# Kernel optimization log

Hardware: AMD Instinct MI355X
Metric: run time of the kernel (lower is better)

## Reference

```python
import jax, jax.numpy as jnp
import numpy as np

D, H, E, K, DFF = 1024, 16, 8, 2, 4096
B, L, T = 4, 512, 2048
EPS = 1e-5


def _xavier(key, shape):
    fan_in, fan_out = shape[-1], shape[-2]
    a = jnp.sqrt(6.0 / (fan_in + fan_out))
    return jax.random.uniform(key, shape, jnp.float32, -a, a)


def setup_inputs() -> dict:
    key = jax.random.key(0)
    ks = jax.random.split(key, 16)
    inp = {
        'latents': jax.random.normal(ks[0], (B, L, D), jnp.float32),
        'tokens': jax.random.normal(ks[1], (B, T, D), jnp.float32),
        # self-attn
        'sa_ln_g': jnp.ones((D,)), 'sa_ln_b': jnp.zeros((D,)),
        'sa_in_w': _xavier(ks[2], (3 * D, D)), 'sa_in_b': jnp.zeros((3 * D,)),
        'sa_out_w': _xavier(ks[3], (D, D)), 'sa_out_b': jnp.zeros((D,)),
        # cross-attn
        'ca_q_ln_g': jnp.ones((D,)), 'ca_q_ln_b': jnp.zeros((D,)),
        'ca_kv_ln_g': jnp.ones((D,)), 'ca_kv_ln_b': jnp.zeros((D,)),
        'ca_in_w': _xavier(ks[4], (3 * D, D)), 'ca_in_b': jnp.zeros((3 * D,)),
        'ca_out_w': _xavier(ks[5], (D, D)), 'ca_out_b': jnp.zeros((D,)),
        # FuseMoE
        'moe_ln_g': jnp.ones((D,)), 'moe_ln_b': jnp.zeros((D,)),
        'router_w': _xavier(ks[6], (E, D)), 'router_b': jnp.zeros((E,)),
        'e_fc1_w': jax.vmap(lambda k: _xavier(k, (DFF, D)))(jax.random.split(ks[7], E)),
        'e_fc1_b': jnp.zeros((E, DFF)),
        'e_fc2_w': jax.vmap(lambda k: _xavier(k, (D, DFF)))(jax.random.split(ks[8], E)),
        'e_fc2_b': jnp.zeros((E, D)),
    }
    return inp


def _ln(x, g, b):
    m = x.mean(-1, keepdims=True)
    v = ((x - m) ** 2).mean(-1, keepdims=True)
    return (x - m) / jnp.sqrt(v + EPS) * g + b


def _mha(q_in, kv_in, in_w, in_b, out_w, out_b):
    # torch nn.MultiheadAttention (batch_first, no masks, eval)
    wq, wk, wv = jnp.split(in_w, 3, axis=0)
    bq, bk, bv = jnp.split(in_b, 3, axis=0)
    dh = D // H
    def heads(x, w, b):  # [B,S,D] -> [B,H,S,dh]
        y = x @ w.T + b
        return y.reshape(x.shape[0], x.shape[1], H, dh).transpose(0, 2, 1, 3)
    q = heads(q_in, wq, bq)
    k = heads(kv_in, wk, bk)
    v = heads(kv_in, wv, bv)
    scores = jnp.einsum('bhqd,bhkd->bhqk', q, k) / jnp.sqrt(jnp.float32(dh))
    attn = jax.nn.softmax(scores, axis=-1)
    out = jnp.einsum('bhqk,bhkd->bhqd', attn, v)
    out = out.transpose(0, 2, 1, 3).reshape(q_in.shape[0], q_in.shape[1], D)
    return out @ out_w.T + out_b


def _fuse_moe(x, ln_g, ln_b, rw, rb, fc1_w, fc1_b, fc2_w, fc2_b):
    h = _ln(x, ln_g, ln_b)
    logits = h @ rw.T + rb                      # [B,L,E]
    vals, idx = jax.lax.top_k(logits, K)        # [B,L,K]
    gates = jax.nn.softmax(vals, axis=-1)
    N = x.shape[0] * x.shape[1]
    hf = h.reshape(N, D)
    # dense all-expert FFN (faithful to original)
    h1 = jax.nn.gelu(jnp.einsum('nd,efd->enf', hf, fc1_w) + fc1_b[:, None, :], approximate=False)
    eo = jnp.einsum('enf,edf->end', h1, fc2_w) + fc2_b[:, None, :]  # [E,N,D]
    idx_f = idx.reshape(N, K)
    gates_f = gates.reshape(N, K)
    gathered = eo[idx_f, jnp.arange(N)[:, None], :]  # [N,K,D]
    mixed = (gathered * gates_f[..., None]).sum(axis=1).reshape(x.shape)
    return x + mixed


def reference(latents, tokens, sa_ln_g, sa_ln_b, sa_in_w, sa_in_b, sa_out_w, sa_out_b,
              ca_q_ln_g, ca_q_ln_b, ca_kv_ln_g, ca_kv_ln_b, ca_in_w, ca_in_b, ca_out_w, ca_out_b,
              moe_ln_g, moe_ln_b, router_w, router_b, e_fc1_w, e_fc1_b, e_fc2_w, e_fc2_b):
    # self-attn (pre-LN, q=k=v)
    q = _ln(latents, sa_ln_g, sa_ln_b)
    x = latents + _mha(q, q, sa_in_w, sa_in_b, sa_out_w, sa_out_b)
    # cross-attn
    qc = _ln(x, ca_q_ln_g, ca_q_ln_b)
    kv = _ln(tokens, ca_kv_ln_g, ca_kv_ln_b)
    x = x + _mha(qc, kv, ca_in_w, ca_in_b, ca_out_w, ca_out_b)
    # FuseMoE FFN
    return _fuse_moe(x, moe_ln_g, moe_ln_b, router_w, router_b, e_fc1_w, e_fc1_b, e_fc2_w, e_fc2_b)
```

## Files before the change

### kernel.cpp

```cpp
#include <hip/hip_runtime.h>
#include <hip/hip_bf16.h>
#include <math.h>

typedef __hip_bfloat16 bf16;
typedef __bf16 bf16x8v __attribute__((ext_vector_type(8)));
typedef float f32x4 __attribute__((ext_vector_type(4)));
typedef unsigned short us8v __attribute__((ext_vector_type(8)));

#define DD   1024
#define HH   16
#define DHD  64
#define EE   8
#define BB   4
#define LL   512
#define TT   2048
#define DFFD 4096
#define NLAT 2048
#define NTOK 8192
#define NASG 4096

__device__ __forceinline__ float toF(float x) { return x; }
__device__ __forceinline__ float toF(bf16 x) { return __bfloat162float(x); }
__device__ __forceinline__ float us2f(unsigned short u) {
    union { unsigned int i; float f; } v; v.i = ((unsigned int)u) << 16; return v.f;
}
__device__ __forceinline__ unsigned short f2us(float f) {
    bf16 t = __float2bfloat16(f);
    return *(unsigned short*)&t;
}

__device__ __forceinline__ float block_sum256(float val, float* red) {
    #pragma unroll
    for (int off = 32; off > 0; off >>= 1) val += __shfl_down(val, off);
    if ((threadIdx.x & 63) == 0) red[threadIdx.x >> 6] = val;
    __syncthreads();
    if (threadIdx.x == 0) red[4] = red[0] + red[1] + red[2] + red[3];
    __syncthreads();
    float r = red[4];
    __syncthreads();
    return r;
}

__global__ __launch_bounds__(256) void ln_kernel(
    const float* __restrict__ x, const float* __restrict__ g, const float* __restrict__ b,
    bf16* __restrict__ out)
{
    __shared__ float red[5];
    int row = blockIdx.x;
    int tid = threadIdx.x;
    const float* xr = x + (size_t)row * DD;
    float v[4];
    #pragma unroll
    for (int i = 0; i < 4; ++i) v[i] = xr[tid + i * 256];
    float s = v[0] + v[1] + v[2] + v[3];
    float mean = block_sum256(s, red) * (1.0f / DD);
    float sq = 0.f;
    #pragma unroll
    for (int i = 0; i < 4; ++i) { float d = v[i] - mean; sq += d * d; }
    float var = block_sum256(sq, red) * (1.0f / DD);
    float rstd = rsqrtf(var + 1e-5f);
    bf16* orow = out + (size_t)row * DD;
    #pragma unroll
    for (int i = 0; i < 4; ++i) {
        int c = tid + i * 256;
        orow[c] = __float2bfloat16((v[i] - mean) * rstd * g[c] + b[c]);
    }
}

__global__ __launch_bounds__(256) void mfma_gemm_kernel(
    const bf16* __restrict__ A, const float* __restrict__ W,
    const float* __restrict__ bias,
    bf16* __restrict__ Cb, float* __restrict__ Cf,
    int M, int N, int K,
    const float* __restrict__ res, int act, int split,
    const int* __restrict__ gather,
    const int* __restrict__ seg_off, const int* __restrict__ seg_cnt)
{
    int m_base = 0, mrows = M;
    if (seg_off) {
        int e = blockIdx.z;
        m_base = seg_off[e];
        mrows  = seg_cnt[e];
        W    += (size_t)e * N * K;
        bias += (size_t)e * N;
    }
    const int m0 = blockIdx.y * 128;
    if (m0 >= mrows) return;
    const int n0 = blockIdx.x * 128;

    __shared__ bf16 As[4][128][8];
    __shared__ bf16 Wh[4][128][8];
    __shared__ bf16 Wl[4][128][8];

    const int tid  = threadIdx.x;
    const int wid  = tid >> 6;
    const int lane = tid & 63;
    const int lg   = lane >> 4;
    const int l16  = lane & 15;
    const int mb   = (wid >> 1) * 64;
    const int nb   = (wid & 1) * 64;

    const int srow  = tid >> 1;
    const int shalf = tid & 1;
    const int kg0   = shalf * 2;

    const bool a_ok = (m0 + srow) < mrows;
    const unsigned short* aptr = nullptr;
    if (a_ok) {
        int grow = m_base + m0 + srow;
        int asrc = gather ? gather[grow] : grow;
        aptr = (const unsigned short*)(A + (size_t)asrc * K + shalf * 16);
    }
    const float* wptr = W + (size_t)(n0 + srow) * K + shalf * 16;

    f32x4 acc[4][4] = {};

    for (int k0 = 0; k0 < K; k0 += 32) {
        us8v av0 = {0,0,0,0,0,0,0,0}, av1 = {0,0,0,0,0,0,0,0};
        if (a_ok) {
            av0 = *(const us8v*)(aptr + k0);
            av1 = *(const us8v*)(aptr + k0 + 8);
        }
        float4 w0 = *(const float4*)(wptr + k0);
        float4 w1 = *(const float4*)(wptr + k0 + 4);
        float4 w2 = *(const float4*)(wptr + k0 + 8);
        float4 w3 = *(const float4*)(wptr + k0 + 12);

        us8v hi0, hi1, lo0, lo1;
        {
            const float fw[16] = {w0.x, w0.y, w0.z, w0.w, w1.x, w1.y, w1.z, w1.w,
                                  w2.x, w2.y, w2.z, w2.w, w3.x, w3.y, w3.z, w3.w};
            #pragma unroll
            for (int j = 0; j < 8; ++j) {
                unsigned short h0 = f2us(fw[j]);
                unsigned short h1 = f2us(fw[j + 8]);
                hi0[j] = h0; hi1[j] = h1;
                lo0[j] = f2us(fw[j] - us2f(h0));
                lo1[j] = f2us(fw[j + 8] - us2f(h1));
            }
        }
        *(us8v*)&As[kg0][srow][0]     = av0;
        *(us8v*)&As[kg0 + 1][srow][0] = av1;
        *(us8v*)&Wh[kg0][srow][0]     = hi0;
        *(us8v*)&Wh[kg0 + 1][srow][0] = hi1;
        if (split) {
            *(us8v*)&Wl[kg0][srow][0]     = lo0;
            *(us8v*)&Wl[kg0 + 1][srow][0] = lo1;
        }
        __syncthreads();

        bf16x8v af[4], wf[4];
        #pragma unroll
        for (int i = 0; i < 4; ++i) af[i] = *(const bf16x8v*)&As[lg][mb + i * 16 + l16][0];
        if (split) {
            bf16x8v wlf[4];
            #pragma unroll
            for (int j = 0; j < 4; ++j) wlf[j] = *(const bf16x8v*)&Wl[lg][nb + j * 16 + l16][0];
            #pragma unroll
            for (int i = 0; i < 4; ++i)
                #pragma unroll
                for (int j = 0; j < 4; ++j)
                    acc[i][j] = __builtin_amdgcn_mfma_f32_16x16x32_bf16(af[i], wlf[j], acc[i][j], 0, 0, 0);
        }
        #pragma unroll
        for (int j = 0; j < 4; ++j) wf[j] = *(const bf16x8v*)&Wh[lg][nb + j * 16 + l16][0];
        #pragma unroll
        for (int i = 0; i < 4; ++i)
            #pragma unroll
            for (int j = 0; j < 4; ++j)
                acc[i][j] = __builtin_amdgcn_mfma_f32_16x16x32_bf16(af[i], wf[j], acc[i][j], 0, 0, 0);
        __syncthreads();
    }

    #pragma unroll
    for (int i = 0; i < 4; ++i) {
        #pragma unroll
        for (int r = 0; r < 4; ++r) {
            int mm = m0 + mb + i * 16 + lg * 4 + r;
            if (mm >= mrows) continue;
            size_t crow = (size_t)(m_base + mm);
            #pragma unroll
            for (int j = 0; j < 4; ++j) {
                int nn = n0 + nb + j * 16 + l16;
                float v = acc[i][j][r] + bias[nn];
                if (act == 1) v = 0.5f * v * (1.0f + erff(v * 0.70710678118654752f));
                if (res) v += res[crow * (size_t)N + nn];
                if (Cb) Cb[crow * (size_t)N + nn] = __float2bfloat16(v);
                else    Cf[crow * (size_t)N + nn] = v;
            }
        }
    }
}

__global__ __launch_bounds__(256) void attn_mfma_kernel(
    const bf16* __restrict__ Q, int ldq, int qoff,
    const bf16* __restrict__ KV, int ldk, int koff, int voff,
    bf16* __restrict__ O, int Lq, int Tk)
{
    __shared__ bf16 Qs[64][72];
    __shared__ bf16 Ks[32][72];
    __shared__ bf16 Vs[64][40];
    __shared__ bf16 Psh[4][16][40];
    __shared__ bf16 Psl[4][16][40];

    const int nqb = Lq >> 6;
    const int qb  = blockIdx.x % nqb;
    const int h   = (blockIdx.x / nqb) % HH;
    const int b   = blockIdx.x / (nqb * HH);

    const int tid  = threadIdx.x;
    const int wq   = tid >> 6;
    const int lane = tid & 63;
    const int lg   = lane >> 4;
    const int l16  = lane & 15;

    {
        const int row = tid >> 2;
        const int c0  = (tid & 3) * 16;
        const unsigned short* src = (const unsigned short*)
            (Q + (size_t)(b * Lq + qb * 64 + row) * ldq + qoff + h * DHD + c0);
        #pragma unroll
        for (int hf = 0; hf < 2; ++hf) {
            us8v v = *(const us8v*)(src + hf * 8);
            us8v o;
            #pragma unroll
            for (int j = 0; j < 8; ++j) o[j] = f2us(us2f(v[j]) * 0.125f);
            *(us8v*)&Qs[row][c0 + hf * 8] = o;
        }
    }
    __syncthreads();

    const int qrow = wq * 16 + l16;
    const bf16x8v fQ0 = *(const bf16x8v*)&Qs[qrow][lg * 8];
    const bf16x8v fQ1 = *(const bf16x8v*)&Qs[qrow][32 + lg * 8];

    float m = -1e30f, lsum = 0.f;
    f32x4 Of[4] = {};

    const size_t kvbase = (size_t)b * Tk * ldk;
    const int kst_k = tid >> 3;
    const int kst_c = (tid & 7) * 8;
    const int vst_k = (tid & 15) * 2;
    const int vst_d = (tid >> 4) * 4;

    for (int t0 = 0; t0 < Tk; t0 += 32) {
        {
            const bf16* ks = KV + kvbase + (size_t)(t0 + kst_k) * ldk + koff + h * DHD + kst_c;
            *(float4*)&Ks[kst_k][kst_c] = *(const float4*)ks;
        }
        {
            const bf16* vsrc = KV + kvbase + (size_t)(t0 + vst_k) * ldk + voff + h * DHD + vst_d;
            ushort4 a = *(const ushort4*)vsrc;
            ushort4 c = *(const ushort4*)(vsrc + ldk);
            unsigned int w;
            w = (unsigned)a.x | ((unsigned)c.x << 16); *(unsigned*)&Vs[vst_d + 0][vst_k] = w;
            w = (unsigned)a.y | ((unsigned)c.y << 16); *(unsigned*)&Vs[vst_d + 1][vst_k] = w;
            w = (unsigned)a.z | ((unsigned)c.z << 16); *(unsigned*)&Vs[vst_d + 2][vst_k] = w;
            w = (unsigned)a.w | ((unsigned)c.w << 16); *(unsigned*)&Vs[vst_d + 3][vst_k] = w;
        }
        __syncthreads();

        f32x4 st0 = {}, st1 = {};
        {
            const bf16x8v k00 = *(const bf16x8v*)&Ks[l16][lg * 8];
            const bf16x8v k10 = *(const bf16x8v*)&Ks[16 + l16][lg * 8];
            const bf16x8v k01 = *(const bf16x8v*)&Ks[l16][32 + lg * 8];
            const bf16x8v k11 = *(const bf16x8v*)&Ks[16 + l16][32 + lg * 8];
            st0 = __builtin_amdgcn_mfma_f32_16x16x32_bf16(k00, fQ0, st0, 0, 0, 0);
            st1 = __builtin_amdgcn_mfma_f32_16x16x32_bf16(k10, fQ0, st1, 0, 0, 0);
            st0 = __builtin_amdgcn_mfma_f32_16x16x32_bf16(k01, fQ1, st0, 0, 0, 0);
            st1 = __builtin_amdgcn_mfma_f32_16x16x32_bf16(k11, fQ1, st1, 0, 0, 0);
        }

        float cm = fmaxf(fmaxf(fmaxf(st0[0], st0[1]), fmaxf(st0[2], st0[3])),
                         fmaxf(fmaxf(st1[0], st1[1]), fmaxf(st1[2], st1[3])));
        cm = fmaxf(cm, __shfl_xor(cm, 16));
        cm = fmaxf(cm, __shfl_xor(cm, 32));
        const float nm = fmaxf(m, cm);
        float p0[4], p1[4];
        float ps = 0.f;
        #pragma unroll
        for (int r = 0; r < 4; ++r) { p0[r] = expf(st0[r] - nm); ps += p0[r]; }
        #pragma unroll
        for (int r = 0; r < 4; ++r) { p1[r] = expf(st1[r] - nm); ps += p1[r]; }
        ps += __shfl_xor(ps, 16);
        ps += __shfl_xor(ps, 32);
        const float alpha = expf(m - nm);
        lsum = lsum * alpha + ps;
        m = nm;

        ushort4 h0, h1, lo0, lo1;
        #pragma unroll
        for (int r = 0; r < 4; ++r) {
            unsigned short hh = f2us(p0[r]);
            ((unsigned short*)&h0)[r]  = hh;
            ((unsigned short*)&lo0)[r] = f2us(p0[r] - us2f(hh));
        }
        #pragma unroll
        for (int r = 0; r < 4; ++r) {
            unsigned short hh = f2us(p1[r]);
            ((unsigned short*)&h1)[r]  = hh;
            ((unsigned short*)&lo1)[r] = f2us(p1[r] - us2f(hh));
        }
        *(ushort4*)&Psh[wq][l16][lg * 4]      = h0;
        *(ushort4*)&Psh[wq][l16][16 + lg * 4] = h1;
        *(ushort4*)&Psl[wq][l16][lg * 4]      = lo0;
        *(ushort4*)&Psl[wq][l16][16 + lg * 4] = lo1;

        #pragma unroll
        for (int r = 0; r < 4; ++r) {
            const float ar = __shfl(alpha, lg * 4 + r);
            Of[0][r] *= ar; Of[1][r] *= ar; Of[2][r] *= ar; Of[3][r] *= ar;
        }

        __syncthreads();

        const bf16x8v pah = *(const bf16x8v*)&Psh[wq][l16][lg * 8];
        const bf16x8v pal = *(const bf16x8v*)&Psl[wq][l16][lg * 8];
        #pragma unroll
        for (int bb = 0; bb < 4; ++bb) {
            const bf16x8v bv = *(const bf16x8v*)&Vs[bb * 16 + l16][lg * 8];
            Of[bb] = __builtin_amdgcn_mfma_f32_16x16x32_bf16(pal, bv, Of[bb], 0, 0, 0);
            Of[bb] = __builtin_amdgcn_mfma_f32_16x16x32_bf16(pah, bv, Of[bb], 0, 0, 0);
        }
        __syncthreads();
    }

    #pragma unroll
    for (int r = 0; r < 4; ++r) {
        const float inv = 1.0f / __shfl(lsum, lg * 4 + r);
        const int grow = b * Lq + qb * 64 + wq * 16 + lg * 4 + r;
        bf16* orow = O + (size_t)grow * DD + h * DHD;
        #pragma unroll
        for (int bb = 0; bb < 4; ++bb)
            orow[bb * 16 + l16] = __float2bfloat16(Of[bb][r] * inv);
    }
}

__global__ __launch_bounds__(64) void router_kernel(
    const float* __restrict__ X2,
    const float* __restrict__ g, const float* __restrict__ b,
    const float* __restrict__ rw, const float* __restrict__ rb,
    float* __restrict__ gates, int* __restrict__ ebuf, int* __restrict__ counts)
{
    int n = blockIdx.x;
    int lane = threadIdx.x;
    const float* xr = X2 + (size_t)n * DD;

    float v[16];
    #pragma unroll
    for (int i = 0; i < 16; ++i) v[i] = xr[lane + i * 64];

    float s = 0.f;
    #pragma unroll
    for (int i = 0; i < 16; ++i) s += v[i];
    #pragma unroll
    for (int off = 32; off > 0; off >>= 1) s += __shfl_xor(s, off);
    float mean = s * (1.0f / DD);

    float sq = 0.f;
    #pragma unroll
    for (int i = 0; i < 16; ++i) { float d = v[i] - mean; sq += d * d; }
    #pragma unroll
    for (int off = 32; off > 0; off >>= 1) sq += __shfl_xor(sq, off);
    float rstd = rsqrtf(sq * (1.0f / DD) + 1e-5f);

    float h[16];
    #pragma unroll
    for (int i = 0; i < 16; ++i) {
        int c = lane + i * 64;
        h[i] = (v[i] - mean) * rstd * g[c] + b[c];
    }

    float logit[EE];
    #pragma unroll
    for (int e = 0; e < EE; ++e) {
        const float* wr = rw + (size_t)e * DD;
        float p = 0.f;
        #pragma unroll
        for (int i = 0; i < 16; ++i) p += h[i] * wr[lane + i * 64];
        #pragma unroll
        for (int off = 32; off > 0; off >>= 1) p += __shfl_xor(p, off);
        logit[e] = p;
    }

    if (lane == 0) {
        #pragma unroll
        for (int e = 0; e < EE; ++e) logit[e] += rb[e];
        int i0 = 0;
        #pragma unroll
        for (int e = 1; e < EE; ++e) if (logit[e] > logit[i0]) i0 = e;
        int i1 = -1;
        #pragma unroll
        for (int e = 0; e < EE; ++e) {
            if (e == i0) continue;
            if (i1 < 0 || logit[e] > logit[i1]) i1 = e;
        }
        float ex = expf(logit[i1] - logit[i0]);
        float inv = 1.0f / (1.0f + ex);
        gates[2 * n + 0] = inv;
        gates[2 * n + 1] = ex * inv;
        ebuf[2 * n + 0] = i0;
        ebuf[2 * n + 1] = i1;
        atomicAdd(&counts[i0], 1);
        atomicAdd(&counts[i1], 1);
    }
}

__global__ void zero8_kernel(int* __restrict__ p) {
    if (threadIdx.x < EE) p[threadIdx.x] = 0;
}

__global__ void prefix_kernel(const int* __restrict__ counts,
                              int* __restrict__ seg_off, int* __restrict__ cursors) {
    if (threadIdx.x == 0) {
        int acc = 0;
        for (int e = 0; e < EE; ++e) { seg_off[e] = acc; cursors[e] = acc; acc += counts[e]; }
    }
}

__global__ __launch_bounds__(256) void scatter_kernel(
    const int* __restrict__ ebuf, int* __restrict__ cursors,
    int* __restrict__ tok_list, int* __restrict__ r_of)
{
    int n = blockIdx.x * 256 + threadIdx.x;
    if (n < NLAT) {
        for (int k = 0; k < 2; ++k) {
            int e = ebuf[2 * n + k];
            int r = atomicAdd(&cursors[e], 1);
            tok_list[r] = n;
            r_of[2 * n + k] = r;
        }
    }
}

__global__ __launch_bounds__(256) void mix_kernel(
    const float* __restrict__ X2, const bf16* __restrict__ EOUT,
    const float* __restrict__ gates, const int* __restrict__ r_of,
    float* __restrict__ out)
{
    int id = blockIdx.x * 256 + threadIdx.x;
    int n = id >> 10;
    int d = id & 1023;
    float v = X2[id]
            + gates[2 * n + 0] * toF(EOUT[(size_t)r_of[2 * n + 0] * DD + d])
            + gates[2 * n + 1] * toF(EOUT[(size_t)r_of[2 * n + 1] * DD + d]);
    out[id] = v;
}

extern "C" void kernel_launch(void* const* d_in, const int* in_sizes, int n_in,
                              void* d_out, int out_size, void* d_ws, size_t ws_size,
                              hipStream_t stream)
{
    const float* latents  = (const float*)d_in[0];
    const float* tokens   = (const float*)d_in[1];
    const float* sa_ln_g  = (const float*)d_in[2];
    const float* sa_ln_b  = (const float*)d_in[3];
    const float* sa_in_w  = (const float*)d_in[4];
    const float* sa_in_b  = (const float*)d_in[5];
    const float* sa_out_w = (const float*)d_in[6];
    const float* sa_out_b = (const float*)d_in[7];
    const float* ca_q_ln_g  = (const float*)d_in[8];
    const float* ca_q_ln_b  = (const float*)d_in[9];
    const float* ca_kv_ln_g = (const float*)d_in[10];
    const float* ca_kv_ln_b = (const float*)d_in[11];
    const float* ca_in_w  = (const float*)d_in[12];
    const float* ca_in_b  = (const float*)d_in[13];
    const float* ca_out_w = (const float*)d_in[14];
    const float* ca_out_b = (const float*)d_in[15];
    const float* moe_ln_g = (const float*)d_in[16];
    const float* moe_ln_b = (const float*)d_in[17];
    const float* router_w = (const float*)d_in[18];
    const float* router_b = (const float*)d_in[19];
    const float* e_fc1_w  = (const float*)d_in[20];
    const float* e_fc1_b  = (const float*)d_in[21];
    const float* e_fc2_w  = (const float*)d_in[22];
    const float* e_fc2_b  = (const float*)d_in[23];

    char* base = (char*)d_ws;
    const size_t MB = (size_t)1 << 20;
    float* X1   = (float*)(base + 0 * MB);
    float* X2   = (float*)(base + 8 * MB);
    bf16*  H    = (bf16*) (base + 16 * MB);
    bf16*  AO   = (bf16*) (base + 20 * MB);
    bf16*  QCA  = (bf16*) (base + 24 * MB);
    bf16*  KVLN = (bf16*) (base + 28 * MB);
    bf16*  EOUT = (bf16*) (base + 28 * MB);
    bf16*  KVCA = (bf16*) (base + 44 * MB);
    bf16*  QKV  = (bf16*) (base + 44 * MB);
    bf16*  H1   = (bf16*) (base + 44 * MB);
    float* GATES = (float*)(base + 76 * MB);
    int* ebuf     = (int*)(base + 76 * MB + 16384);
    int* tok_list = ebuf + NASG;
    int* r_of     = tok_list + NASG;
    int* counts   = r_of + NASG;
    int* seg_off  = counts + EE;
    int* cursors  = seg_off + EE;

    ln_kernel<<<NLAT, 256, 0, stream>>>(latents, sa_ln_g, sa_ln_b, H);
    {
        dim3 g(3072 / 128, NLAT / 128, 1);
        mfma_gemm_kernel<<<g, 256, 0, stream>>>(H, sa_in_w, sa_in_b, QKV, nullptr,
                                                NLAT, 3072, DD,
                                                nullptr, 0, 1, nullptr, nullptr, nullptr);
    }
    attn_mfma_kernel<<<BB * HH * (LL / 64), 256, 0, stream>>>(
        QKV, 3072, 0, QKV, 3072, 1024, 2048, AO, LL, LL);
    {
        dim3 g(DD / 128, NLAT / 128, 1);
        mfma_gemm_kernel<<<g, 256, 0, stream>>>(AO, sa_out_w, sa_out_b, nullptr, X1,
                                                NLAT, DD, DD,
                                                latents, 0, 1, nullptr, nullptr, nullptr);
    }
    ln_kernel<<<NLAT, 256, 0, stream>>>(X1, ca_q_ln_g, ca_q_ln_b, H);
    ln_kernel<<<NTOK, 256, 0, stream>>>(tokens, ca_kv_ln_g, ca_kv_ln_b, KVLN);
    {
        dim3 g(DD / 128, NLAT / 128, 1);
        mfma_gemm_kernel<<<g, 256, 0, stream>>>(H, ca_in_w, ca_in_b, QCA, nullptr,
                                                NLAT, DD, DD,
                                                nullptr, 0, 1, nullptr, nullptr, nullptr);
    }
    {
        dim3 g(2048 / 128, NTOK / 128, 1);
        mfma_gemm_kernel<<<g, 256, 0, stream>>>(KVLN, ca_in_w + (size_t)1024 * DD, ca_in_b + 1024,
                                                KVCA, nullptr, NTOK, 2048, DD,
                                                nullptr, 0, 1, nullptr, nullptr, nullptr);
    }
    attn_mfma_kernel<<<BB * HH * (LL / 64), 256, 0, stream>>>(
        QCA, 1024, 0, KVCA, 2048, 0, 1024, AO, LL, TT);
    {
        dim3 g(DD / 128, NLAT / 128, 1);
        mfma_gemm_kernel<<<g, 256, 0, stream>>>(AO, ca_out_w, ca_out_b, nullptr, X2,
                                                NLAT, DD, DD,
                                                X1, 0, 1, nullptr, nullptr, nullptr);
    }
    ln_kernel<<<NLAT, 256, 0, stream>>>(X2, moe_ln_g, moe_ln_b, H);
    zero8_kernel<<<1, 64, 0, stream>>>(counts);
    router_kernel<<<NLAT, 64, 0, stream>>>(X2, moe_ln_g, moe_ln_b, router_w, router_b,
                                           GATES, ebuf, counts);
    prefix_kernel<<<1, 64, 0, stream>>>(counts, seg_off, cursors);
    scatter_kernel<<<NLAT / 256, 256, 0, stream>>>(ebuf, cursors, tok_list, r_of);
    {
        dim3 g(DFFD / 128, NLAT / 128, EE);
        mfma_gemm_kernel<<<g, 256, 0, stream>>>(H, e_fc1_w, e_fc1_b, H1, nullptr,
                                                0, DFFD, DD,
                                                nullptr, 1, 0, tok_list, seg_off, counts);
    }
    {
        dim3 g(DD / 128, NLAT / 128, EE);
        mfma_gemm_kernel<<<g, 256, 0, stream>>>(H1, e_fc2_w, e_fc2_b, EOUT, nullptr,
                                                0, DD, DFFD,
                                                nullptr, 0, 0, nullptr, seg_off, counts);
    }
    mix_kernel<<<(NLAT * DD) / 256, 256, 0, stream>>>(X2, EOUT, GATES, r_of, (float*)d_out);
}
```

Before: 1.212 ms.

## Prefetch next K tile into registers and template GEMM on split mode

The GEMM main loop is restructured to load the next 32-wide K tile from global memory into registers while MFMAs run on the current tile in shared memory. This is register-level software pipelining meant to hide global load latency. The split flag becomes a template parameter, so the non-split MoE GEMMs drop the low-part shared buffer and its conversion work. The cost is more registers per thread, which may lower occupancy, and the loop now assumes K is a multiple of 64.

```diff
diff --git a/kernel.cpp b/kernel.cpp
--- a/kernel.cpp
+++ b/kernel.cpp
@@ -67,12 +67,13 @@
     }
 }
 
-__global__ __launch_bounds__(256) void mfma_gemm_kernel(
+template<int SPLIT>
+__global__ __launch_bounds__(256) void mfma_gemm_t(
     const bf16* __restrict__ A, const float* __restrict__ W,
     const float* __restrict__ bias,
     bf16* __restrict__ Cb, float* __restrict__ Cf,
     int M, int N, int K,
-    const float* __restrict__ res, int act, int split,
+    const float* __restrict__ res, int act,
     const int* __restrict__ gather,
     const int* __restrict__ seg_off, const int* __restrict__ seg_cnt)
 {
@@ -88,9 +89,11 @@
     if (m0 >= mrows) return;
     const int n0 = blockIdx.x * 128;
 
-    __shared__ bf16 As[4][128][8];
-    __shared__ bf16 Wh[4][128][8];
-    __shared__ bf16 Wl[4][128][8];
+    constexpr int HALF = 4 * 128 * 8;
+    __shared__ bf16 smem[(SPLIT ? 3 : 2) * HALF];
+    bf16* AsB = smem;
+    bf16* WhB = smem + HALF;
+    bf16* WlB = smem + 2 * HALF;
 
     const int tid  = threadIdx.x;
     const int wid  = tid >> 6;
@@ -115,21 +118,27 @@
 
     f32x4 acc[4][4] = {};
 
-    for (int k0 = 0; k0 < K; k0 += 32) {
-        us8v av0 = {0,0,0,0,0,0,0,0}, av1 = {0,0,0,0,0,0,0,0};
+    auto load_tile = [&](us8v (&ar)[2], float4 (&wr)[4], int kk) {
         if (a_ok) {
-            av0 = *(const us8v*)(aptr + k0);
-            av1 = *(const us8v*)(aptr + k0 + 8);
-        }
-        float4 w0 = *(const float4*)(wptr + k0);
-        float4 w1 = *(const float4*)(wptr + k0 + 4);
-        float4 w2 = *(const float4*)(wptr + k0 + 8);
-        float4 w3 = *(const float4*)(wptr + k0 + 12);
-
-        us8v hi0, hi1, lo0, lo1;
-        {
-            const float fw[16] = {w0.x, w0.y, w0.z, w0.w, w1.x, w1.y, w1.z, w1.w,
-                                  w2.x, w2.y, w2.z, w2.w, w3.x, w3.y, w3.z, w3.w};
+            ar[0] = *(const us8v*)(aptr + kk);
+            ar[1] = *(const us8v*)(aptr + kk + 8);
+        }
+        wr[0] = *(const float4*)(wptr + kk);
+        wr[1] = *(const float4*)(wptr + kk + 4);
+        wr[2] = *(const float4*)(wptr + kk + 8);
+        wr[3] = *(const float4*)(wptr + kk + 12);
+    };
+
+    auto store_tile = [&](const us8v (&ar)[2], const float4 (&wr)[4]) {
+        *(us8v*)(AsB + ((size_t)kg0 * 128 + srow) * 8)       = ar[0];
+        *(us8v*)(AsB + ((size_t)(kg0 + 1) * 128 + srow) * 8) = ar[1];
+        const float fw[16] = {wr[0].x, wr[0].y, wr[0].z, wr[0].w,
+                              wr[1].x, wr[1].y, wr[1].z, wr[1].w,
+                              wr[2].x, wr[2].y, wr[2].z, wr[2].w,
+                              wr[3].x, wr[3].y, wr[3].z, wr[3].w};
+        us8v hi0, hi1;
+        if constexpr (SPLIT) {
+            us8v lo0, lo1;
             #pragma unroll
             for (int j = 0; j < 8; ++j) {
                 unsigned short h0 = f2us(fw[j]);
@@ -138,37 +147,58 @@
                 lo0[j] = f2us(fw[j] - us2f(h0));
                 lo1[j] = f2us(fw[j + 8] - us2f(h1));
             }
-        }
-        *(us8v*)&As[kg0][srow][0]     = av0;
-        *(us8v*)&As[kg0 + 1][srow][0] = av1;
-        *(us8v*)&Wh[kg0][srow][0]     = hi0;
-        *(us8v*)&Wh[kg0 + 1][srow][0] = hi1;
-        if (split) {
-            *(us8v*)&Wl[kg0][srow][0]     = lo0;
-            *(us8v*)&Wl[kg0 + 1][srow][0] = lo1;
-        }
-        __syncthreads();
-
-        bf16x8v af[4], wf[4];
-        #pragma unroll
-        for (int i = 0; i < 4; ++i) af[i] = *(const bf16x8v*)&As[lg][mb + i * 16 + l16][0];
-        if (split) {
-            bf16x8v wlf[4];
+            *(us8v*)(WlB + ((size_t)kg0 * 128 + srow) * 8)       = lo0;
+            *(us8v*)(WlB + ((size_t)(kg0 + 1) * 128 + srow) * 8) = lo1;
+        } else {
             #pragma unroll
-            for (int j = 0; j < 4; ++j) wlf[j] = *(const bf16x8v*)&Wl[lg][nb + j * 16 + l16][0];
+            for (int j = 0; j < 8; ++j) {
+                hi0[j] = f2us(fw[j]);
+                hi1[j] = f2us(fw[j + 8]);
+            }
+        }
+        *(us8v*)(WhB + ((size_t)kg0 * 128 + srow) * 8)       = hi0;
+        *(us8v*)(WhB + ((size_t)(kg0 + 1) * 128 + srow) * 8) = hi1;
+    };
+
+    auto compute = [&]() {
+        bf16x8v af[4];
+        #pragma unroll
+        for (int i = 0; i < 4; ++i)
+            af[i] = *(const bf16x8v*)(AsB + ((size_t)lg * 128 + mb + i * 16 + l16) * 8);
+        if constexpr (SPLIT) {
+            #pragma unroll
+            for (int j = 0; j < 4; ++j) {
+                bf16x8v wlf = *(const bf16x8v*)(WlB + ((size_t)lg * 128 + nb + j * 16 + l16) * 8);
+                #pragma unroll
+                for (int i = 0; i < 4; ++i)
+                    acc[i][j] = __builtin_amdgcn_mfma_f32_16x16x32_bf16(af[i], wlf, acc[i][j], 0, 0, 0);
+            }
+        }
+        #pragma unroll
+        for (int j = 0; j < 4; ++j) {
+            bf16x8v wf = *(const bf16x8v*)(WhB + ((size_t)lg * 128 + nb + j * 16 + l16) * 8);
             #pragma unroll
             for (int i = 0; i < 4; ++i)
-                #pragma unroll
-                for (int j = 0; j < 4; ++j)
-                    acc[i][j] = __builtin_amdgcn_mfma_f32_16x16x32_bf16(af[i], wlf[j], acc[i][j], 0, 0, 0);
-        }
-        #pragma unroll
-        for (int j = 0; j < 4; ++j) wf[j] = *(const bf16x8v*)&Wh[lg][nb + j * 16 + l16][0];
-        #pragma unroll
-        for (int i = 0; i < 4; ++i)
-            #pragma unroll
-            for (int j = 0; j < 4; ++j)
-                acc[i][j] = __builtin_amdgcn_mfma_f32_16x16x32_bf16(af[i], wf[j], acc[i][j], 0, 0, 0);
+                acc[i][j] = __builtin_amdgcn_mfma_f32_16x16x32_bf16(af[i], wf, acc[i][j], 0, 0, 0);
+        }
+    };
+
+    us8v a0[2] = {}, a1[2] = {};
+    float4 w0r[4], w1r[4];
+    load_tile(a0, w0r, 0);
+
+    for (int k0 = 0; k0 < K; k0 += 64) {
+        store_tile(a0, w0r);
+        __syncthreads();
+        load_tile(a1, w1r, k0 + 32);
+        compute();
+        __syncthreads();
+
+        store_tile(a1, w1r);
+        __syncthreads();
+        const int kn = k0 + 64;
+        if (kn < K) load_tile(a0, w0r, kn);
+        compute();
         __syncthreads();
     }
 
@@ -500,39 +530,39 @@
     ln_kernel<<<NLAT, 256, 0, stream>>>(latents, sa_ln_g, sa_ln_b, H);
     {
         dim3 g(3072 / 128, NLAT / 128, 1);
-        mfma_gemm_kernel<<<g, 256, 0, stream>>>(H, sa_in_w, sa_in_b, QKV, nullptr,
-                                                NLAT, 3072, DD,
-                                                nullptr, 0, 1, nullptr, nullptr, nullptr);
+        mfma_gemm_t<1><<<g, 256, 0, stream>>>(H, sa_in_w, sa_in_b, QKV, nullptr,
+                                              NLAT, 3072, DD,
+                                              nullptr, 0, nullptr, nullptr, nullptr);
     }
     attn_mfma_kernel<<<BB * HH * (LL / 64), 256, 0, stream>>>(
         QKV, 3072, 0, QKV, 3072, 1024, 2048, AO, LL, LL);
     {
         dim3 g(DD / 128, NLAT / 128, 1);
-        mfma_gemm_kernel<<<g, 256, 0, stream>>>(AO, sa_out_w, sa_out_b, nullptr, X1,
-                                                NLAT, DD, DD,
-                                                latents, 0, 1, nullptr, nullptr, nullptr);
+        mfma_gemm_t<1><<<g, 256, 0, stream>>>(AO, sa_out_w, sa_out_b, nullptr, X1,
+                                              NLAT, DD, DD,
+                                              latents, 0, nullptr, nullptr, nullptr);
     }
     ln_kernel<<<NLAT, 256, 0, stream>>>(X1, ca_q_ln_g, ca_q_ln_b, H);
     ln_kernel<<<NTOK, 256, 0, stream>>>(tokens, ca_kv_ln_g, ca_kv_ln_b, KVLN);
     {
         dim3 g(DD / 128, NLAT / 128, 1);
-        mfma_gemm_kernel<<<g, 256, 0, stream>>>(H, ca_in_w, ca_in_b, QCA, nullptr,
-                                                NLAT, DD, DD,
-                                                nullptr, 0, 1, nullptr, nullptr, nullptr);
+        mfma_gemm_t<1><<<g, 256, 0, stream>>>(H, ca_in_w, ca_in_b, QCA, nullptr,
+                                              NLAT, DD, DD,
+                                              nullptr, 0, nullptr, nullptr, nullptr);
     }
     {
         dim3 g(2048 / 128, NTOK / 128, 1);
-        mfma_gemm_kernel<<<g, 256, 0, stream>>>(KVLN, ca_in_w + (size_t)1024 * DD, ca_in_b + 1024,
-                                                KVCA, nullptr, NTOK, 2048, DD,
-                                                nullptr, 0, 1, nullptr, nullptr, nullptr);
+        mfma_gemm_t<1><<<g, 256, 0, stream>>>(KVLN, ca_in_w + (size_t)1024 * DD, ca_in_b + 1024,
+                                              KVCA, nullptr, NTOK, 2048, DD,
+                                              nullptr, 0, nullptr, nullptr, nullptr);
     }
     attn_mfma_kernel<<<BB * HH * (LL / 64), 256, 0, stream>>>(
         QCA, 1024, 0, KVCA, 2048, 0, 1024, AO, LL, TT);
     {
         dim3 g(DD / 128, NLAT / 128, 1);
-        mfma_gemm_kernel<<<g, 256, 0, stream>>>(AO, ca_out_w, ca_out_b, nullptr, X2,
-                                                NLAT, DD, DD,
-                                                X1, 0, 1, nullptr, nullptr, nullptr);
+        mfma_gemm_t<1><<<g, 256, 0, stream>>>(AO, ca_out_w, ca_out_b, nullptr, X2,
+                                              NLAT, DD, DD,
+                                              X1, 0, nullptr, nullptr, nullptr);
     }
     ln_kernel<<<NLAT, 256, 0, stream>>>(X2, moe_ln_g, moe_ln_b, H);
     zero8_kernel<<<1, 64, 0, stream>>>(counts);
@@ -542,15 +572,15 @@
     scatter_kernel<<<NLAT / 256, 256, 0, stream>>>(ebuf, cursors, tok_list, r_of);
     {
         dim3 g(DFFD / 128, NLAT / 128, EE);
-        mfma_gemm_kernel<<<g, 256, 0, stream>>>(H, e_fc1_w, e_fc1_b, H1, nullptr,
-                                                0, DFFD, DD,
-                                                nullptr, 1, 0, tok_list, seg_off, counts);
+        mfma_gemm_t<0><<<g, 256, 0, stream>>>(H, e_fc1_w, e_fc1_b, H1, nullptr,
+                                              0, DFFD, DD,
+                                              nullptr, 1, tok_list, seg_off, counts);
     }
     {
         dim3 g(DD / 128, NLAT / 128, EE);
-        mfma_gemm_kernel<<<g, 256, 0, stream>>>(H1, e_fc2_w, e_fc2_b, EOUT, nullptr,
-                                                0, DD, DFFD,
-                                                nullptr, 0, 0, nullptr, seg_off, counts);
+        mfma_gemm_t<0><<<g, 256, 0, stream>>>(H1, e_fc2_w, e_fc2_b, EOUT, nullptr,
+                                              0, DD, DFFD,
+                                              nullptr, 0, nullptr, seg_off, counts);
     }
     mix_kernel<<<(NLAT * DD) / 256, 256, 0, stream>>>(X2, EOUT, GATES, r_of, (float*)d_out);
 }
```

Result: faster. 1.175 ms (-3.0%).
